# Kernel optimization log

Hardware: AMD Instinct MI355X
Metric: run time of the kernel (lower is better)

Reference implementation:

```python
import jax, jax.numpy as jnp
import numpy as np

B, T, D = 4, 2048, 512
H, HS = 8, 64            # n_head, head_size
E, K = 8, 2              # num_experts, top_k
CAP = int(B * T * K / E * 1.0)  # expert capacity = 2048
EPS = 1e-5


def setup_inputs() -> dict:
    key = jax.random.key(0)
    ks = jax.random.split(key, 16)
    s = lambda k, shp, fan: jax.random.normal(k, shp, jnp.float32) * (fan ** -0.5)
    return {
        "x": jax.random.normal(ks[0], (B, T, D), jnp.float32),
        "ln1_g": jnp.ones((D,), jnp.float32), "ln1_b": jnp.zeros((D,), jnp.float32),
        "Wq": s(ks[1], (H, D, HS), D), "Wk": s(ks[2], (H, D, HS), D), "Wv": s(ks[3], (H, D, HS), D),
        "Wo": s(ks[4], (D, D), D), "bo": jnp.zeros((D,), jnp.float32),
        "ln2_g": jnp.ones((D,), jnp.float32), "ln2_b": jnp.zeros((D,), jnp.float32),
        "Wg": s(ks[5], (D, E), D), "bg": jnp.zeros((E,), jnp.float32),
        "Wn": s(ks[6], (D, E), D), "bn": jnp.zeros((E,), jnp.float32),
        "W1": s(ks[7], (E, D, 4 * D), D), "b1": jnp.zeros((E, 4 * D), jnp.float32),
        "W2": s(ks[8], (E, 4 * D, D), 4 * D), "b2": jnp.zeros((E, D), jnp.float32),
    }


def _ln(x, g, b):
    m = jnp.mean(x, -1, keepdims=True)
    v = jnp.var(x, -1, keepdims=True)
    return (x - m) * jax.lax.rsqrt(v + EPS) * g + b


def _attn(h, Wq, Wk, Wv, Wo, bo):
    q = jnp.einsum('btd,hde->bhte', h, Wq)
    k = jnp.einsum('btd,hde->bhte', h, Wk)
    v = jnp.einsum('btd,hde->bhte', h, Wv)
    # NOTE: source scales by C**-0.5 with C = n_embed (not head_size)
    wei = jnp.einsum('bhte,bhse->bhts', q, k) * (D ** -0.5)
    causal = jnp.tril(jnp.ones((T, T), bool))
    wei = jnp.where(causal, wei, -jnp.inf)
    wei = jax.nn.softmax(wei, axis=-1)
    out = jnp.einsum('bhts,bhse->bhte', wei, v)              # [B,H,T,HS]
    out = out.transpose(0, 2, 1, 3).reshape(B, T, D)          # concat heads
    return out @ Wo + bo


def _moe(h, Wg, bg, Wn, bn, W1, b1, W2, b2):
    logits = h @ Wg + bg
    noise_logits = h @ Wn + bn
    noise = jax.random.normal(jax.random.key(42), logits.shape, logits.dtype) * jax.nn.softplus(noise_logits)
    noisy = logits + noise
    vals, idx = jax.lax.top_k(noisy, K)                       # [B,T,K]
    # softmax over -inf-masked sparse logits == softmax over top-k values, scattered
    gates = (jax.nn.softmax(vals, -1)[..., None] * jax.nn.one_hot(idx, E, dtype=h.dtype)).sum(-2)  # [B,T,E]
    flat_x = h.reshape(-1, D)
    flat_g = gates.reshape(-1, E)
    flat_idx = idx.reshape(-1, K)
    N = flat_x.shape[0]
    mask = (flat_idx[None] == jnp.arange(E)[:, None, None]).any(-1)   # [E,N]
    rank = jnp.cumsum(mask, axis=1) - 1
    keep = mask & (rank < CAP)                                 # first CAP tokens per expert
    slot = jnp.where(keep, rank, CAP)
    tok = jnp.arange(N, dtype=jnp.int32)

    def build(s, kp):
        buf = jnp.zeros(CAP + 1, jnp.int32).at[s].set(tok)
        vb = jnp.zeros(CAP + 1, bool).at[s].set(kp)
        return buf[:CAP], vb[:CAP]

    idx_buf, valid = jax.vmap(build)(slot, keep)               # [E,CAP]
    xg = flat_x[idx_buf]                                       # [E,CAP,D]
    mid = jax.nn.relu(jnp.einsum('ecd,edf->ecf', xg, W1) + b1[:, None, :])
    out = jnp.einsum('ecf,efd->ecd', mid, W2) + b2[:, None, :]
    gate_sel = flat_g[idx_buf, jnp.arange(E)[:, None]]         # [E,CAP]
    w = out * (gate_sel * valid.astype(h.dtype))[..., None]
    upd = jnp.zeros_like(flat_x).at[idx_buf.reshape(-1)].add(w.reshape(-1, D))
    return upd.reshape(h.shape)


def reference(x, ln1_g, ln1_b, Wq, Wk, Wv, Wo, bo, ln2_g, ln2_b,
              Wg, bg, Wn, bn, W1, b1, W2, b2):
    x = x + _attn(_ln(x, ln1_g, ln1_b), Wq, Wk, Wv, Wo, bo)
    x = x + _moe(_ln(x, ln2_g, ln2_b), Wg, bg, Wn, bn, W1, b1, W2, b2)
    return x
```

## Files before the change

kernel.cpp:

```cpp
#include <hip/hip_runtime.h>
#include <math.h>

#define TSEQ 2048
#define DD   512
#define NH   8
#define HSZ  64
#define NE   8
#define NTOK 8192
#define CAPK 2048
#define FF   2048

typedef __bf16 bf16x8 __attribute__((ext_vector_type(8)));
typedef float  f32x4  __attribute__((ext_vector_type(4)));
typedef unsigned int u32;
typedef u32 u32x2 __attribute__((ext_vector_type(2)));
typedef short s16x4 __attribute__((ext_vector_type(4)));

#define WAITVM(N) asm volatile("s_waitcnt vmcnt(" #N ")" ::: "memory")

__device__ __forceinline__ void gload16(const void* g, void* l){
  __builtin_amdgcn_global_load_lds((const __attribute__((address_space(1))) u32*)g,
                                   (__attribute__((address_space(3))) u32*)l, 16, 0, 0);
}

__device__ __forceinline__ u32 pkbf(float a, float b){
  unsigned short ua = __builtin_bit_cast(unsigned short, (__bf16)a);
  unsigned short ub = __builtin_bit_cast(unsigned short, (__bf16)b);
  return (u32)ua | ((u32)ub << 16);
}

__device__ __forceinline__ s16x4 mk4(u32 a, u32 b){
  u32x2 t; t[0] = a; t[1] = b;
  return __builtin_bit_cast(s16x4, t);
}

__device__ __forceinline__ unsigned rotl32(unsigned x, int r){ return (x<<r)|(x>>(32-r)); }

__device__ __forceinline__ void threefry2x32(unsigned c0, unsigned c1, unsigned &o0, unsigned &o1){
  const unsigned k0 = 0u, k1 = 42u;
  const unsigned k2 = k0 ^ k1 ^ 0x1BD11BDAu;
  unsigned x0 = c0 + k0, x1 = c1 + k1;
#define TFR(rot) { x0 += x1; x1 = rotl32(x1, rot); x1 ^= x0; }
  TFR(13) TFR(15) TFR(26) TFR(6)   x0 += k1; x1 += k2 + 1u;
  TFR(17) TFR(29) TFR(16) TFR(24)  x0 += k2; x1 += k0 + 2u;
  TFR(13) TFR(15) TFR(26) TFR(6)   x0 += k0; x1 += k1 + 3u;
  TFR(17) TFR(29) TFR(16) TFR(24)  x0 += k1; x1 += k2 + 4u;
  TFR(13) TFR(15) TFR(26) TFR(6)   x0 += k2; x1 += k0 + 5u;
#undef TFR
  o0 = x0; o1 = x1;
}

__device__ __forceinline__ float erfinv_f(float x){
  float w = -log1pf(-x*x);
  float p;
  if (w < 5.0f){
    w -= 2.5f;
    p = 2.81022636e-08f;
    p = fmaf(p,w, 3.43273939e-07f);
    p = fmaf(p,w,-3.5233877e-06f);
    p = fmaf(p,w,-4.39150654e-06f);
    p = fmaf(p,w, 0.00021858087f);
    p = fmaf(p,w,-0.00125372503f);
    p = fmaf(p,w,-0.00417768164f);
    p = fmaf(p,w, 0.246640727f);
    p = fmaf(p,w, 1.50140941f);
  } else {
    w = sqrtf(w) - 3.0f;
    p = -0.000200214257f;
    p = fmaf(p,w, 0.000100950558f);
    p = fmaf(p,w, 0.00134934322f);
    p = fmaf(p,w,-0.00367342844f);
    p = fmaf(p,w, 0.00573950773f);
    p = fmaf(p,w,-0.0076224613f);
    p = fmaf(p,w, 0.00943887047f);
    p = fmaf(p,w, 1.00167406f);
    p = fmaf(p,w, 2.83297682f);
  }
  return p * x;
}

__global__ __launch_bounds__(256) void ln_split(const float* __restrict__ x,
    const float* __restrict__ gw, const float* __restrict__ bw,
    __bf16* __restrict__ ohi, __bf16* __restrict__ olo)
{
  int row  = blockIdx.x*4 + threadIdx.y;
  int lane = threadIdx.x;
  const float* xr = x + (size_t)row*DD;
  float4 a = *(const float4*)(xr + lane*4);
  float4 c = *(const float4*)(xr + 256 + lane*4);
  float s  = a.x+a.y+a.z+a.w + c.x+c.y+c.z+c.w;
  float ss = a.x*a.x+a.y*a.y+a.z*a.z+a.w*a.w + c.x*c.x+c.y*c.y+c.z*c.z+c.w*c.w;
  #pragma unroll
  for (int off = 32; off; off >>= 1){ s += __shfl_xor(s, off); ss += __shfl_xor(ss, off); }
  float m   = s * (1.0f/DD);
  float var = ss * (1.0f/DD) - m*m;
  float r   = 1.0f / sqrtf(var + 1e-5f);
  float4 g1 = *(const float4*)(gw + lane*4);
  float4 b1 = *(const float4*)(bw + lane*4);
  float4 g2 = *(const float4*)(gw + 256 + lane*4);
  float4 b2 = *(const float4*)(bw + 256 + lane*4);
  float f1[4], f2[4];
  f1[0]=(a.x-m)*r*g1.x+b1.x; f1[1]=(a.y-m)*r*g1.y+b1.y; f1[2]=(a.z-m)*r*g1.z+b1.z; f1[3]=(a.w-m)*r*g1.w+b1.w;
  f2[0]=(c.x-m)*r*g2.x+b2.x; f2[1]=(c.y-m)*r*g2.y+b2.y; f2[2]=(c.z-m)*r*g2.z+b2.z; f2[3]=(c.w-m)*r*g2.w+b2.w;
  __bf16 h1v[4] __attribute__((aligned(8))), l1v[4] __attribute__((aligned(8)));
  __bf16 h2v[4] __attribute__((aligned(8))), l2v[4] __attribute__((aligned(8)));
  #pragma unroll
  for (int j = 0; j < 4; ++j){
    __bf16 hb = (__bf16)f1[j]; h1v[j]=hb; l1v[j]=(__bf16)(f1[j]-(float)hb);
    __bf16 hc = (__bf16)f2[j]; h2v[j]=hc; l2v[j]=(__bf16)(f2[j]-(float)hc);
  }
  size_t base = (size_t)row*DD + lane*4;
  *(uint2*)(ohi + base)       = *(const uint2*)h1v;
  *(uint2*)(olo + base)       = *(const uint2*)l1v;
  *(uint2*)(ohi + base + 256) = *(const uint2*)h2v;
  *(uint2*)(olo + base + 256) = *(const uint2*)l2v;
}

__global__ __launch_bounds__(256) void pack_qkv_split(const float* __restrict__ Wq,
    const float* __restrict__ Wk, const float* __restrict__ Wv,
    __bf16* __restrict__ dhi, __bf16* __restrict__ dlo)
{
  __shared__ float t[64][65];
  int z = blockIdx.y;
  int kt = blockIdx.x*64;
  int sel = z >> 3, hh = z & 7;
  const float* W = (sel==0 ? Wq : (sel==1 ? Wk : Wv)) + (size_t)hh*DD*HSZ;
  int tid = threadIdx.x;
  int r = tid>>2, c0 = (tid&3)*16;
  #pragma unroll
  for (int j = 0; j < 16; j += 4){
    float4 v = *(const float4*)&W[(size_t)(kt+r)*HSZ + c0 + j];
    t[r][c0+j]=v.x; t[r][c0+j+1]=v.y; t[r][c0+j+2]=v.z; t[r][c0+j+3]=v.w;
  }
  __syncthreads();
  __bf16 hb[16] __attribute__((aligned(32)));
  __bf16 lb[16] __attribute__((aligned(32)));
  #pragma unroll
  for (int j = 0; j < 16; ++j){
    float f = t[c0+j][r];
    __bf16 h = (__bf16)f; hb[j]=h; lb[j]=(__bf16)(f-(float)h);
  }
  size_t off = (size_t)(z*64 + r)*512 + kt + c0;
  *(uint4*)(dhi+off) = ((const uint4*)hb)[0]; *(uint4*)(dhi+off+8) = ((const uint4*)hb)[1];
  *(uint4*)(dlo+off) = ((const uint4*)lb)[0]; *(uint4*)(dlo+off+8) = ((const uint4*)lb)[1];
}

__global__ __launch_bounds__(256) void transp_split(const float* __restrict__ src,
    __bf16* __restrict__ dhi, __bf16* __restrict__ dlo, int Ms, int Ns)
{
  __shared__ float t[64][65];
  int nt = blockIdx.x*64, mt = blockIdx.y*64;
  int tid = threadIdx.x;
  int r = tid>>2, c0 = (tid&3)*16;
  #pragma unroll
  for (int j = 0; j < 16; j += 4){
    float4 v = *(const float4*)&src[(size_t)(mt+r)*Ns + nt + c0 + j];
    t[r][c0+j]=v.x; t[r][c0+j+1]=v.y; t[r][c0+j+2]=v.z; t[r][c0+j+3]=v.w;
  }
  __syncthreads();
  __bf16 hb[16] __attribute__((aligned(32)));
  __bf16 lb[16] __attribute__((aligned(32)));
  #pragma unroll
  for (int j = 0; j < 16; ++j){
    float f = t[c0+j][r];
    __bf16 h = (__bf16)f; hb[j]=h; lb[j]=(__bf16)(f-(float)h);
  }
  size_t off = (size_t)(nt + r)*Ms + mt + c0;
  *(uint4*)(dhi+off) = ((const uint4*)hb)[0]; *(uint4*)(dhi+off+8) = ((const uint4*)hb)[1];
  *(uint4*)(dlo+off) = ((const uint4*)lb)[0]; *(uint4*)(dlo+off+8) = ((const uint4*)lb)[1];
}

template<int BIAS, int RES>
__global__ __launch_bounds__(256) void gemm_mfma3(
    const __bf16* __restrict__ Ahi, const __bf16* __restrict__ Alo,
    const __bf16* __restrict__ Bhi, const __bf16* __restrict__ Blo,
    const float* __restrict__ bias, const float* __restrict__ res,
    float* __restrict__ C, int M, int N, int K)
{
  __shared__ __bf16 AsH[2][4096];
  __shared__ __bf16 AsL[2][4096];
  __shared__ __bf16 BsH[2][4096];
  __shared__ __bf16 BsL[2][4096];
  int m0 = blockIdx.y*128, n0 = blockIdx.x*128;
  int tid = threadIdx.x;
  int w = tid>>6, l = tid&63;
  int wm = w>>1, wn = w&1;
  int srow = w*32 + (l>>2);
  int skb  = (l&3)<<4;
  const char* agh = (const char*)(Ahi + (size_t)(m0+srow)*K) + skb;
  const char* agl = (const char*)(Alo + (size_t)(m0+srow)*K) + skb;
  const char* bgh = (const char*)(Bhi + (size_t)(n0+srow)*K) + skb;
  const char* bgl = (const char*)(Blo + (size_t)(n0+srow)*K) + skb;
  size_t r16 = (size_t)16*K*sizeof(__bf16);

  f32x4 acc[4][4] = {};
  int rl = l & 15, kh = l >> 4;
  const __bf16* abh = &AsH[0][(wm*64 + rl)*32 + kh*8];
  const __bf16* abl = &AsL[0][(wm*64 + rl)*32 + kh*8];
  const __bf16* bbh = &BsH[0][(wn*64 + rl)*32 + kh*8];
  const __bf16* bbl = &BsL[0][(wn*64 + rl)*32 + kh*8];

  auto STAGE = [&](int bb, int kt){
    size_t o = (size_t)kt*64;
    gload16(agh+o,     &AsH[bb][w*1024]);
    gload16(agh+o+r16, &AsH[bb][w*1024+512]);
    gload16(agl+o,     &AsL[bb][w*1024]);
    gload16(agl+o+r16, &AsL[bb][w*1024+512]);
    gload16(bgh+o,     &BsH[bb][w*1024]);
    gload16(bgh+o+r16, &BsH[bb][w*1024+512]);
    gload16(bgl+o,     &BsL[bb][w*1024]);
    gload16(bgl+o+r16, &BsL[bb][w*1024+512]);
  };

  int nkt = K >> 5;
  STAGE(0, 0);
  for (int kt = 0; kt < nkt; ++kt){
    int bb = kt & 1;
    if (kt + 1 < nkt){ STAGE(bb^1, kt+1); WAITVM(8); }
    else             { WAITVM(0); }
    __builtin_amdgcn_s_barrier();
    bf16x8 afh[4], afl[4], bfh[4], bfl[4];
    #pragma unroll
    for (int i = 0; i < 4; ++i){
      afh[i] = *(const bf16x8*)(abh + bb*4096 + i*512);
      afl[i] = *(const bf16x8*)(abl + bb*4096 + i*512);
      bfh[i] = *(const bf16x8*)(bbh + bb*4096 + i*512);
      bfl[i] = *(const bf16x8*)(bbl + bb*4096 + i*512);
    }
    #pragma unroll
    for (int fm = 0; fm < 4; ++fm)
      #pragma unroll
      for (int fn = 0; fn < 4; ++fn){
        acc[fm][fn] = __builtin_amdgcn_mfma_f32_16x16x32_bf16(afh[fm], bfl[fn], acc[fm][fn], 0, 0, 0);
        acc[fm][fn] = __builtin_amdgcn_mfma_f32_16x16x32_bf16(afl[fm], bfh[fn], acc[fm][fn], 0, 0, 0);
        acc[fm][fn] = __builtin_amdgcn_mfma_f32_16x16x32_bf16(afh[fm], bfh[fn], acc[fm][fn], 0, 0, 0);
      }
    __builtin_amdgcn_s_barrier();
  }

  int ccol = l & 15, cr = (l >> 4) * 4;
  #pragma unroll
  for (int fn = 0; fn < 4; ++fn){
    int n = n0 + wn*64 + fn*16 + ccol;
    float bv = BIAS ? bias[n] : 0.0f;
    #pragma unroll
    for (int fm = 0; fm < 4; ++fm){
      int mb = m0 + wm*64 + fm*16 + cr;
      #pragma unroll
      for (int r = 0; r < 4; ++r){
        float v = acc[fm][fn][r] + bv;
        if (RES) v += res[(size_t)(mb+r)*N + n];
        C[(size_t)(mb+r)*N + n] = v;
// ... 13 lines not shown
  int flat = blockIdx.x;
  int e = flat & ((1<<EBITS)-1);
  int tile = flat >> EBITS;
  int n0 = (tile & ((1<<LOGN)-1)) * 128;
  int m0 = (tile >> LOGN) * 128;
  const __bf16* Be = Bt + (size_t)e*N*K;
  const float*  be = bias + (size_t)e*N;
  int tid = threadIdx.x;
  int w = tid>>6, l = tid&63;
  int wm = w>>1, wn = w&1;
  int srow = w*32 + (l>>2);
  int skb  = (l&3)<<4;
  const char* ag;
  if (GATHER){
    int tok = idxb[e*CAPK + m0 + srow];
    ag = (const char*)(A + (size_t)tok*K) + skb;
  } else {
    ag = (const char*)(A + (size_t)e*M*K + (size_t)(m0 + srow)*K) + skb;
  }
  const char* bg = (const char*)(Be + (size_t)(n0 + srow)*K) + skb;
  size_t r16;
  if (GATHER){
    int tok2 = idxb[e*CAPK + m0 + srow + 16];
    r16 = (size_t)((const char*)(A + (size_t)tok2*K) + skb - ag);
  } else {
    r16 = (size_t)16*K*sizeof(__bf16);
  }

  f32x4 acc[4][4] = {};
  int rl = l & 15, kh = l >> 4;
  const __bf16* abase = &Asl[0][(wm*64 + rl)*32 + kh*8];
  const __bf16* bbase = &Bsl[0][(wn*64 + rl)*32 + kh*8];

  size_t br16 = (size_t)16*K*sizeof(__bf16);
  auto STAGE = [&](int bb, int kt){
    size_t o = (size_t)kt*64;
    gload16(ag+o,      &Asl[bb][w*1024]);
    gload16(ag+o+r16,  &Asl[bb][w*1024+512]);
    gload16(bg+o,      &Bsl[bb][w*1024]);
    gload16(bg+o+br16, &Bsl[bb][w*1024+512]);
  };

  int nkt = K >> 5;
  STAGE(0, 0);
  for (int kt = 0; kt < nkt; ++kt){
    int bb = kt & 1;
    if (kt + 1 < nkt){ STAGE(bb^1, kt+1); WAITVM(4); }
    else             { WAITVM(0); }
    __builtin_amdgcn_s_barrier();
    bf16x8 af[4], bf[4];
    #pragma unroll
    for (int i = 0; i < 4; ++i){
      af[i] = *(const bf16x8*)(abase + bb*4096 + i*512);
      bf[i] = *(const bf16x8*)(bbase + bb*4096 + i*512);
    }
    #pragma unroll
    for (int fm = 0; fm < 4; ++fm)
      #pragma unroll
      for (int fn = 0; fn < 4; ++fn)
        acc[fm][fn] = __builtin_amdgcn_mfma_f32_16x16x32_bf16(af[fm], bf[fn], acc[fm][fn], 0, 0, 0);
    __builtin_amdgcn_s_barrier();
  }

  int ccol = l & 15, cr = (l >> 4) * 4;
  char* Ce = (char*)Cv + (size_t)e*M*N*(STORE_BF16 ? 2 : 4);
  #pragma unroll
  for (int fn = 0; fn < 4; ++fn){
    int n = n0 + wn*64 + fn*16 + ccol;
    float bv = be[n];
    #pragma unroll
    for (int fm = 0; fm < 4; ++fm){
      int mb = m0 + wm*64 + fm*16 + cr;
      #pragma unroll
      for (int r = 0; r < 4; ++r){
        float v = acc[fm][fn][r] + bv;
        if (RELU) v = fmaxf(v, 0.f);
        if (STORE_BF16) ((__bf16*)Ce)[(size_t)(mb+r)*N + n] = (__bf16)v;
        else            ((float*)Ce)[(size_t)(mb+r)*N + n] = v;
      }
    }
  }
}

__global__ __launch_bounds__(256) void transp_conv(const float* __restrict__ src,
    __bf16* __restrict__ dst, int Ms, int Ns)
{
  __shared__ __bf16 t[64][72];
  int e = blockIdx.z;
  const float* s = src + (size_t)e*Ms*Ns;
  __bf16* d = dst + (size_t)e*Ms*Ns;
  int mt = blockIdx.y*64, nt = blockIdx.x*64;
  int tid = threadIdx.x;
  int r = tid>>2, c0 = (tid&3)*16;
  #pragma unroll
  for (int j = 0; j < 16; j += 4){
    float4 v = *(const float4*)&s[(size_t)(mt+r)*Ns + nt + c0 + j];
    t[r][c0+j]   = (__bf16)v.x; t[r][c0+j+1] = (__bf16)v.y;
    t[r][c0+j+2] = (__bf16)v.z; t[r][c0+j+3] = (__bf16)v.w;
  }
  __syncthreads();
  __bf16 tmp[16] __attribute__((aligned(32)));
  #pragma unroll
  for (int j = 0; j < 16; ++j) tmp[j] = t[c0+j][r];
  uint4* dp = (uint4*)&d[(size_t)(nt+r)*Ms + mt + c0];
  dp[0] = ((const uint4*)tmp)[0];
  dp[1] = ((const uint4*)tmp)[1];
}

__global__ __launch_bounds__(256) void convert_kv(const float* __restrict__ qkv,
    __bf16* __restrict__ khi, __bf16* __restrict__ klo,
    __bf16* __restrict__ vthi, __bf16* __restrict__ vtlo)
{
  int t0 = blockIdx.x*64;
  int bh = blockIdx.y;
  int b = bh >> 3, h = bh & 7;
  int tid = threadIdx.x;
  {
    int r = tid >> 2, e0 = (tid & 3) * 16;
    const float* src = qkv + ((size_t)(b*TSEQ + t0 + r))*1536 + 512 + h*64 + e0;
    __bf16 hi[16] __attribute__((aligned(16)));
    __bf16 lo[16] __attribute__((aligned(16)));
    #pragma unroll
    for (int j = 0; j < 16; j += 4){
      float4 v = *(const float4*)(src + j);
      float f[4] = {v.x, v.y, v.z, v.w};
      #pragma unroll
      for (int q = 0; q < 4; ++q){
        __bf16 hb = (__bf16)f[q];
        hi[j+q] = hb; lo[j+q] = (__bf16)(f[q] - (float)hb);
      }
    }
    size_t off = ((size_t)(bh*TSEQ + t0 + r))*64 + e0;
    *(uint4*)(khi + off)     = ((const uint4*)hi)[0];
    *(uint4*)(khi + off + 8) = ((const uint4*)hi)[1];
    *(uint4*)(klo + off)     = ((const uint4*)lo)[0];
    *(uint4*)(klo + off + 8) = ((const uint4*)lo)[1];
  }
  {
    int key0 = (tid & 15) * 4, e0 = (tid >> 4) * 4;
    float4 v[4];
    #pragma unroll
    for (int j = 0; j < 4; ++j)
      v[j] = *(const float4*)(qkv + ((size_t)(b*TSEQ + t0 + key0 + j))*1536 + 1024 + h*64 + e0);
    float col[4][4];
    col[0][0]=v[0].x; col[0][1]=v[1].x; col[0][2]=v[2].x; col[0][3]=v[3].x;
    col[1][0]=v[0].y; col[1][1]=v[1].y; col[1][2]=v[2].y; col[1][3]=v[3].y;
    col[2][0]=v[0].z; col[2][1]=v[1].z; col[2][2]=v[2].z; col[2][3]=v[3].z;
    col[3][0]=v[0].w; col[3][1]=v[1].w; col[3][2]=v[2].w; col[3][3]=v[3].w;
    #pragma unroll
    for (int kk = 0; kk < 4; ++kk){
      __bf16 hi[4] __attribute__((aligned(8)));
      __bf16 lo[4] __attribute__((aligned(8)));
      #pragma unroll
      for (int j = 0; j < 4; ++j){
        __bf16 hb = (__bf16)col[kk][j];
        hi[j] = hb; lo[j] = (__bf16)(col[kk][j] - (float)hb);
      }
      size_t off = ((size_t)(bh*64 + e0 + kk))*TSEQ + t0 + key0;
      *(uint2*)(vthi + off) = *(const uint2*)hi;
      *(uint2*)(vtlo + off) = *(const uint2*)lo;
    }
  }
}

__global__ __launch_bounds__(512) void attn_mfma(const float* __restrict__ qkv,
    const __bf16* __restrict__ khi_g, const __bf16* __restrict__ klo_g,
    const __bf16* __restrict__ vthi_g, const __bf16* __restrict__ vtlo_g,
    __bf16* __restrict__ ahi, __bf16* __restrict__ alo)
{
  __shared__ __align__(16) char ldsbuf[65536];
  int bh = blockIdx.x;
  int qtA = blockIdx.y, qtB = 15 - qtA;
  int b = bh >> 3, h = bh & 7;
  int tid = threadIdx.x;
  int w = tid >> 6, l = tid & 63;
  int g = l >> 4, r = l & 15;
  const float qsc = 0.04419417382415922f * 1.4426950408889634f;

  int qb[2]; qb[0] = qtA*128 + w*16; qb[1] = qtB*128 + (7-w)*16;
  int kdiag[2]; kdiag[0] = qb[0] >> 6; kdiag[1] = qb[1] >> 6;

  bf16x8 qhi[2][2], qlo[2][2];
  #pragma unroll
  for (int qf = 0; qf < 2; ++qf)
    #pragma unroll
    for (int ks = 0; ks < 2; ++ks){
      const float* src = qkv + ((size_t)(b*TSEQ + qb[qf] + r))*1536 + h*64 + ks*32 + g*8;
      float4 v0 = *(const float4*)src;
      float4 v1 = *(const float4*)(src + 4);
      float f[8] = {v0.x,v0.y,v0.z,v0.w,v1.x,v1.y,v1.z,v1.w};
      bf16x8 hi, lo;
      #pragma unroll
      for (int i = 0; i < 8; ++i){
        float fs = f[i] * qsc;
        __bf16 hb = (__bf16)fs;
        hi[i] = hb; lo[i] = (__bf16)(fs - (float)hb);
      }
      qhi[qf][ks] = hi; qlo[qf][ks] = lo;
    }

  f32x4 ot[4][2] = {};
  float m_r[2] = {-INFINITY, -INFINITY};
  float l_r[2] = {0.f, 0.f};

  int nkt = 2*qtB + 2;
  size_t kbase = (size_t)bh*TSEQ*64;
  size_t vbase = (size_t)bh*64*TSEQ;

  auto STAGE = [&](int buf, int kt){
    int row = tid >> 3, cc = tid & 7;
    int sw = (cc ^ (row & 7)) * 8;
    char* d = ldsbuf + buf*32768 + (w << 10);
    gload16(khi_g  + kbase + (size_t)(kt*64 + row)*64 + sw, d);
    gload16(klo_g  + kbase + (size_t)(kt*64 + row)*64 + sw, d + 8192);
    gload16(vthi_g + vbase + (size_t)row*TSEQ + kt*64 + sw,  d + 16384);
    gload16(vtlo_g + vbase + (size_t)row*TSEQ + kt*64 + sw,  d + 24576);
  };

  STAGE(0, 0);

  for (int kt = 0; kt < nkt; ++kt){
    int buf = kt & 1;
    if (kt + 1 < nkt){ STAGE(buf ^ 1, kt + 1); WAITVM(4); }
    else             { WAITVM(0); }
    __builtin_amdgcn_s_barrier();

    bool act[2];
    act[0] = (kt <= kdiag[0]);
    act[1] = (kt <= kdiag[1]);

    const char* K0 = ldsbuf + buf*32768;
    const char* K1 = K0 + 8192;
    const char* V0 = K0 + 16384;
    const char* V1 = K0 + 24576;

    f32x4 s[4][2] = {};
    #pragma unroll
    for (int kf = 0; kf < 4; ++kf){
      int rowk = kf*16 + r;
      int rsw = (rowk & 7) << 4;
      #pragma unroll
      for (int ks = 0; ks < 2; ++ks){
        int off = rowk*128 + ((((ks*4 + g) << 4)) ^ rsw);
        bf16x8 khf = *(const bf16x8*)(K0 + off);
        bf16x8 klf = *(const bf16x8*)(K1 + off);
        #pragma unroll
        for (int qf = 0; qf < 2; ++qf){
          if (act[qf]){
            s[kf][qf] = __builtin_amdgcn_mfma_f32_16x16x32_bf16(khf, qlo[qf][ks], s[kf][qf], 0,0,0);
            s[kf][qf] = __builtin_amdgcn_mfma_f32_16x16x32_bf16(klf, qhi[qf][ks], s[kf][qf], 0,0,0);
            s[kf][qf] = __builtin_amdgcn_mfma_f32_16x16x32_bf16(khf, qhi[qf][ks], s[kf][qf], 0,0,0);
          }
        }
      }
    }

    u32 phi[4][2][2], plo[4][2][2];
    #pragma unroll
    for (int qf = 0; qf < 2; ++qf){
      if (act[qf]){
        int q = qb[qf] + r;
        float p[4][4];
        float mx = -INFINITY;
        if (kt == kdiag[qf]){
          #pragma unroll
          for (int kf = 0; kf < 4; ++kf)
            #pragma unroll
            for (int e = 0; e < 4; ++e){
              int key = kt*64 + kf*16 + g*4 + e;
              float sv = (key <= q) ? s[kf][qf][e] : -INFINITY;
              p[kf][e] = sv;
              mx = fmaxf(mx, sv);
            }
        } else {
          #pragma unroll
          for (int kf = 0; kf < 4; ++kf)
            #pragma unroll
            for (int e = 0; e < 4; ++e){
              float sv = s[kf][qf][e];
              p[kf][e] = sv;
              mx = fmaxf(mx, sv);
            }
        }
        mx = fmaxf(mx, __shfl_xor(mx, 16));
        mx = fmaxf(mx, __shfl_xor(mx, 32));
        if (__any(mx > m_r[qf])){
          float mn = fmaxf(m_r[qf], mx);
          float fj = exp2f(m_r[qf] - mn);
          m_r[qf] = mn;
          l_r[qf] *= fj;
          #pragma unroll
          for (int ef = 0; ef < 4; ++ef)
            #pragma unroll
            for (int e = 0; e < 4; ++e)
              ot[ef][qf][e] *= fj;
        }
        float ts = 0.f;
        #pragma unroll
        for (int kf = 0; kf < 4; ++kf)
          #pragma unroll
          for (int e = 0; e < 4; ++e){
            float pv = exp2f(p[kf][e] - m_r[qf]);
            p[kf][e] = pv; ts += pv;
          }
        ts += __shfl_xor(ts, 16); ts += __shfl_xor(ts, 32);
        l_r[qf] += ts;
        #pragma unroll
        for (int kf = 0; kf < 4; ++kf){
          __bf16 h0=(__bf16)p[kf][0], h1=(__bf16)p[kf][1], h2=(__bf16)p[kf][2], h3=(__bf16)p[kf][3];
          phi[kf][qf][0] = pkbf(p[kf][0], p[kf][1]);
          phi[kf][qf][1] = pkbf(p[kf][2], p[kf][3]);
          plo[kf][qf][0] = pkbf(p[kf][0]-(float)h0, p[kf][1]-(float)h1);
          plo[kf][qf][1] = pkbf(p[kf][2]-(float)h2, p[kf][3]-(float)h3);
        }
      }
    }

    #pragma unroll
    for (int kf = 0; kf < 4; ++kf){
      #pragma unroll
      for (int ef = 0; ef < 4; ++ef){
        int rowv = ef*16 + r;
        int off = rowv*128 + ((((2*kf + (g>>1)) ^ (rowv & 7)) << 4)) + (g&1)*8;
        s16x4 vh = *(const s16x4*)(V0 + off);
        s16x4 vl = *(const s16x4*)(V1 + off);
        #pragma unroll
        for (int qf = 0; qf < 2; ++qf){
          if (act[qf]){
            s16x4 ph = mk4(phi[kf][qf][0], phi[kf][qf][1]);
            s16x4 pl = mk4(plo[kf][qf][0], plo[kf][qf][1]);
            ot[ef][qf] = __builtin_amdgcn_mfma_f32_16x16x16bf16_1k(vh, pl, ot[ef][qf], 0,0,0);
            ot[ef][qf] = __builtin_amdgcn_mfma_f32_16x16x16bf16_1k(vl, ph, ot[ef][qf], 0,0,0);
            ot[ef][qf] = __builtin_amdgcn_mfma_f32_16x16x16bf16_1k(vh, ph, ot[ef][qf], 0,0,0);
          }
        }
      }
    }
    __builtin_amdgcn_s_barrier();
  }

  float* Osh = (float*)ldsbuf;
  #pragma unroll
  for (int qf = 0; qf < 2; ++qf){
    float inv = 1.0f / l_r[qf];
    int qloc = (qf ? (7-w) : w)*16 + r;
    #pragma unroll
    for (int ef = 0; ef < 4; ++ef)
      #pragma unroll
      for (int e = 0; e < 4; ++e)
        Osh[qloc*68 + ef*16 + g*4 + e] = ot[ef][qf][e] * inv;
    __syncthreads();
    {
      int qt = qf ? qtB : qtA;
      int q = tid >> 2, e0 = (tid & 3)*16;
      const float* srow = Osh + q*68 + e0;
      size_t base = ((size_t)(b*TSEQ + qt*128 + q))*DD + h*64 + e0;
      #pragma unroll
      for (int j = 0; j < 4; ++j){
        float4 v = *(const float4*)(srow + j*4);
        float f[4] = {v.x, v.y, v.z, v.w};
        __bf16 hb[4] __attribute__((aligned(8)));
        __bf16 lb[4] __attribute__((aligned(8)));
        #pragma unroll
        for (int q2 = 0; q2 < 4; ++q2){
          __bf16 h2b = (__bf16)f[q2];
          hb[q2] = h2b; lb[q2] = (__bf16)(f[q2] - (float)h2b);
        }
        *(uint2*)(ahi + base + j*4) = *(const uint2*)hb;
        *(uint2*)(alo + base + j*4) = *(const uint2*)lb;
      }
    }
    __syncthreads();
  }
}

__global__ __launch_bounds__(256) void routerln_kernel(const float* __restrict__ x1,
    const float* __restrict__ gw, const float* __restrict__ bw,
    const float* __restrict__ Wg, const float* __restrict__ bg,
    const float* __restrict__ Wn, const float* __restrict__ bn,
    __bf16* __restrict__ h2b,
    int* __restrict__ idx0, int* __restrict__ idx1,
    float* __restrict__ g0, float* __restrict__ g1)
{
  int wid = threadIdx.x >> 6, lane = threadIdx.x & 63;
  int tok = blockIdx.x*4 + wid;
  const float* xr = x1 + (size_t)tok*DD;
  float4 a = *(const float4*)(xr + lane*4);
  float4 c = *(const float4*)(xr + 256 + lane*4);
  float s  = a.x+a.y+a.z+a.w + c.x+c.y+c.z+c.w;
  float ss = a.x*a.x+a.y*a.y+a.z*a.z+a.w*a.w + c.x*c.x+c.y*c.y+c.z*c.z+c.w*c.w;
  #pragma unroll
  for (int off = 32; off; off >>= 1){ s += __shfl_xor(s, off); ss += __shfl_xor(ss, off); }
  float m   = s * (1.0f/DD);
  float var = ss * (1.0f/DD) - m*m;
  float rr  = 1.0f / sqrtf(var + 1e-5f);
  float4 g1v = *(const float4*)(gw + lane*4);
  float4 b1v = *(const float4*)(bw + lane*4);
  float4 g2v = *(const float4*)(gw + 256 + lane*4);
  float4 b2v = *(const float4*)(bw + 256 + lane*4);
  float f1[4], f2[4];
  f1[0]=(a.x-m)*rr*g1v.x+b1v.x; f1[1]=(a.y-m)*rr*g1v.y+b1v.y; f1[2]=(a.z-m)*rr*g1v.z+b1v.z; f1[3]=(a.w-m)*rr*g1v.w+b1v.w;
  f2[0]=(c.x-m)*rr*g2v.x+b2v.x; f2[1]=(c.y-m)*rr*g2v.y+b2v.y; f2[2]=(c.z-m)*rr*g2v.z+b2v.z; f2[3]=(c.w-m)*rr*g2v.w+b2v.w;
  {
    __bf16 h1v[4] __attribute__((aligned(8)));
    __bf16 h2v[4] __attribute__((aligned(8)));
    #pragma unroll
    for (int j = 0; j < 4; ++j){ h1v[j] = (__bf16)f1[j]; h2v[j] = (__bf16)f2[j]; }
    size_t base = (size_t)tok*DD + lane*4;
    *(uint2*)(h2b + base)       = *(const uint2*)h1v;
    *(uint2*)(h2b + base + 256) = *(const uint2*)h2v;
  }
  float ag[8] = {0,0,0,0,0,0,0,0}, an[8] = {0,0,0,0,0,0,0,0};
  int d1 = lane*4, d2 = 256 + lane*4;
// ... 41 lines not shown
    float dexp = expf(v1 - v0);
    float ssum = 1.0f + dexp;
    idx0[tok] = i0; idx1[tok] = i1;
    g0[tok] = 1.0f/ssum; g1[tok] = dexp/ssum;
  }
}

__global__ __launch_bounds__(256) void route_scan(const int* __restrict__ idx0,
    const int* __restrict__ idx1, int* __restrict__ idx_buf, int* __restrict__ tok_slot)
{
  int e = blockIdx.x, tid = threadIdx.x;
  for (int i = tid; i < CAPK; i += 256) idx_buf[e*CAPK + i] = 0;
  __syncthreads();
  int base = tid * 32;
  int cnt = 0;
  for (int j = 0; j < 32; ++j){ int t = base + j; cnt += (idx0[t]==e || idx1[t]==e) ? 1 : 0; }
  __shared__ int ps[256];
  ps[tid] = cnt; __syncthreads();
  for (int off = 1; off < 256; off <<= 1){
    int add = (tid >= off) ? ps[tid - off] : 0;
    __syncthreads();
    ps[tid] += add;
    __syncthreads();
  }
  int slot = ps[tid] - cnt;
  for (int j = 0; j < 32; ++j){
    int t = base + j;
    int k = (idx0[t]==e) ? 0 : ((idx1[t]==e) ? 1 : -1);
    if (k >= 0){
      if (slot < CAPK){ idx_buf[e*CAPK + slot] = t; tok_slot[t*2 + k] = slot; }
      else            { tok_slot[t*2 + k] = -1; }
      slot++;
    }
  }
}

__global__ __launch_bounds__(128) void combine_kernel(const float* __restrict__ x1,
    const __bf16* __restrict__ eout, const int* __restrict__ idx0, const int* __restrict__ idx1,
    const float* __restrict__ g0, const float* __restrict__ g1,
    const int* __restrict__ tok_slot, float* __restrict__ outp)
{
  int n = blockIdx.x, t = threadIdx.x;
  float4 acc = *(const float4*)(x1 + (size_t)n*DD + t*4);
  #pragma unroll
  for (int k = 0; k < 2; ++k){
    int s = tok_slot[n*2 + k];
    if (s >= 0){
      int e  = (k==0) ? idx0[n] : idx1[n];
      float g = (k==0) ? g0[n] : g1[n];
      __bf16 vb[4] __attribute__((aligned(8)));
      *(uint2*)vb = *(const uint2*)(eout + ((size_t)(e*CAPK + s))*DD + t*4);
      acc.x = fmaf(g, (float)vb[0], acc.x); acc.y = fmaf(g, (float)vb[1], acc.y);
      acc.z = fmaf(g, (float)vb[2], acc.z); acc.w = fmaf(g, (float)vb[3], acc.w);
    }
  }
  *(float4*)(outp + (size_t)n*DD + t*4) = acc;
}

extern "C" void kernel_launch(void* const* d_in, const int* in_sizes, int n_in,
                              void* d_out, int out_size, void* d_ws, size_t ws_size,
                              hipStream_t stream)
{
  const float* x    = (const float*)d_in[0];
  const float* ln1g = (const float*)d_in[1];
  const float* ln1b = (const float*)d_in[2];
  const float* Wq   = (const float*)d_in[3];
  const float* Wk   = (const float*)d_in[4];
  const float* Wv   = (const float*)d_in[5];
  const float* Wo   = (const float*)d_in[6];
  const float* bo   = (const float*)d_in[7];
  const float* ln2g = (const float*)d_in[8];
  const float* ln2b = (const float*)d_in[9];
  const float* Wg   = (const float*)d_in[10];
  const float* bg   = (const float*)d_in[11];
  const float* Wn   = (const float*)d_in[12];
  const float* bn   = (const float*)d_in[13];
  const float* W1   = (const float*)d_in[14];
  const float* b1   = (const float*)d_in[15];
  const float* W2   = (const float*)d_in[16];
  const float* b2   = (const float*)d_in[17];
  float* out = (float*)d_out;
  char* ws = (char*)d_ws;
  const size_t MB = 1u << 20;

  __bf16* h1hi   = (__bf16*)(ws);
  __bf16* h1lo   = (__bf16*)(ws + 8*MB);
  __bf16* attnhi = (__bf16*)(ws);
  __bf16* attnlo = (__bf16*)(ws + 8*MB);
  __bf16* h2b    = (__bf16*)(ws);
  float*  qkv    = (float*)(ws + 16*MB);
  __bf16* W1T    = (__bf16*)(ws + 16*MB);
  __bf16* W2T    = (__bf16*)(ws + 32*MB);
  __bf16* eoutb  = (__bf16*)(ws + 48*MB);
  float*  x1     = (float*)(ws + 64*MB);
  __bf16* Khi    = (__bf16*)(ws + 80*MB);
  __bf16* Klo    = (__bf16*)(ws + 88*MB);
  __bf16* Vthi   = (__bf16*)(ws + 96*MB);
  __bf16* Vtlo   = (__bf16*)(ws + 104*MB);
  __bf16* Bqh    = (__bf16*)(ws + 80*MB);
  __bf16* Bql    = (__bf16*)(ws + 82*MB);
  __bf16* mid    = (__bf16*)(ws + 80*MB);
  __bf16* WoTh   = (__bf16*)(ws + 144*MB);
  __bf16* WoTl   = (__bf16*)(ws + 144*MB + 512*1024);
  char*   smallp = ws + 145*MB;
  int*   idx0     = (int*)smallp;
  int*   idx1     = idx0 + NTOK;
  float* g0       = (float*)(idx1 + NTOK);
  float* g1       = g0 + NTOK;
  int*   tok_slot = (int*)(g1 + NTOK);
  int*   idx_buf  = tok_slot + NTOK*2;

  ln_split<<<dim3(NTOK/4), dim3(64,4), 0, stream>>>(x, ln1g, ln1b, h1hi, h1lo);
  pack_qkv_split<<<dim3(8,24), 256, 0, stream>>>(Wq, Wk, Wv, Bqh, Bql);
  transp_split<<<dim3(8,8), 256, 0, stream>>>(Wo, WoTh, WoTl, DD, DD);
  gemm_mfma3<0,0><<<dim3(12,64), 256, 0, stream>>>(h1hi, h1lo, Bqh, Bql, nullptr, nullptr, qkv, NTOK, 1536, DD);
  convert_kv<<<dim3(TSEQ/64, 32), 256, 0, stream>>>(qkv, Khi, Klo, Vthi, Vtlo);
  attn_mfma<<<dim3(32, 8), 512, 0, stream>>>(qkv, Khi, Klo, Vthi, Vtlo, attnhi, attnlo);
  gemm_mfma3<1,1><<<dim3(4,64), 256, 0, stream>>>(attnhi, attnlo, WoTh, WoTl, bo, x, x1, NTOK, DD, DD);
  routerln_kernel<<<dim3(NTOK/4), 256, 0, stream>>>(x1, ln2g, ln2b, Wg, bg, Wn, bn,
      h2b, idx0, idx1, g0, g1);
  transp_conv<<<dim3(32,8,NE), 256, 0, stream>>>(W1, W1T, DD, FF);
  transp_conv<<<dim3(8,32,NE), 256, 0, stream>>>(W2, W2T, FF, DD);
  route_scan<<<dim3(NE), 256, 0, stream>>>(idx0, idx1, idx_buf, tok_slot);
  gemm_mfma<1,1,1,4,3><<<dim3(8*16*16), 256, 0, stream>>>(
      h2b, W1T, b1, mid, idx_buf, CAPK, FF, DD);
  gemm_mfma<1,0,0,2,3><<<dim3(8*16*4), 256, 0, stream>>>(
      mid, W2T, b2, eoutb, nullptr, CAPK, DD, FF);
  combine_kernel<<<dim3(NTOK), 128, 0, stream>>>(x1, eoutb, idx0, idx1, g0, g1, tok_slot, out);
}
```

Baseline: 385.9 us.

## Use 128-key attention tiles with dynamic LDS and merge prep kernels

The attention kernel now stages 128 keys per iteration instead of 64. That halves the number of loop trips, barriers and softmax rescales, and needs 128KB of dynamic LDS set through hipFuncSetAttribute. The LayerNorm and the QKV/Wo weight packing are merged into one launch, and the W1/W2 transposes into another, to cut launch overhead. The larger tile uses more registers and LDS, which may lower occupancy, and it computes more masked work on the diagonal tile.

```diff
diff --git a/kernel.cpp b/kernel.cpp
--- a/kernel.cpp
+++ b/kernel.cpp
@@ -79,95 +79,92 @@
   return p * x;
 }
 
-__global__ __launch_bounds__(256) void ln_split(const float* __restrict__ x,
-    const float* __restrict__ gw, const float* __restrict__ bw,
-    __bf16* __restrict__ ohi, __bf16* __restrict__ olo)
-{
-  int row  = blockIdx.x*4 + threadIdx.y;
-  int lane = threadIdx.x;
-  const float* xr = x + (size_t)row*DD;
-  float4 a = *(const float4*)(xr + lane*4);
-  float4 c = *(const float4*)(xr + 256 + lane*4);
-  float s  = a.x+a.y+a.z+a.w + c.x+c.y+c.z+c.w;
-  float ss = a.x*a.x+a.y*a.y+a.z*a.z+a.w*a.w + c.x*c.x+c.y*c.y+c.z*c.z+c.w*c.w;
-  #pragma unroll
-  for (int off = 32; off; off >>= 1){ s += __shfl_xor(s, off); ss += __shfl_xor(ss, off); }
-  float m   = s * (1.0f/DD);
-  float var = ss * (1.0f/DD) - m*m;
-  float r   = 1.0f / sqrtf(var + 1e-5f);
-  float4 g1 = *(const float4*)(gw + lane*4);
-  float4 b1 = *(const float4*)(bw + lane*4);
-  float4 g2 = *(const float4*)(gw + 256 + lane*4);
-  float4 b2 = *(const float4*)(bw + 256 + lane*4);
-  float f1[4], f2[4];
-  f1[0]=(a.x-m)*r*g1.x+b1.x; f1[1]=(a.y-m)*r*g1.y+b1.y; f1[2]=(a.z-m)*r*g1.z+b1.z; f1[3]=(a.w-m)*r*g1.w+b1.w;
-  f2[0]=(c.x-m)*r*g2.x+b2.x; f2[1]=(c.y-m)*r*g2.y+b2.y; f2[2]=(c.z-m)*r*g2.z+b2.z; f2[3]=(c.w-m)*r*g2.w+b2.w;
-  __bf16 h1v[4] __attribute__((aligned(8))), l1v[4] __attribute__((aligned(8)));
-  __bf16 h2v[4] __attribute__((aligned(8))), l2v[4] __attribute__((aligned(8)));
-  #pragma unroll
-  for (int j = 0; j < 4; ++j){
-    __bf16 hb = (__bf16)f1[j]; h1v[j]=hb; l1v[j]=(__bf16)(f1[j]-(float)hb);
-    __bf16 hc = (__bf16)f2[j]; h2v[j]=hc; l2v[j]=(__bf16)(f2[j]-(float)hc);
-  }
-  size_t base = (size_t)row*DD + lane*4;
-  *(uint2*)(ohi + base)       = *(const uint2*)h1v;
-  *(uint2*)(olo + base)       = *(const uint2*)l1v;
-  *(uint2*)(ohi + base + 256) = *(const uint2*)h2v;
-  *(uint2*)(olo + base + 256) = *(const uint2*)l2v;
-}
-
-__global__ __launch_bounds__(256) void pack_qkv_split(const float* __restrict__ Wq,
-    const float* __restrict__ Wk, const float* __restrict__ Wv,
-    __bf16* __restrict__ dhi, __bf16* __restrict__ dlo)
+__global__ __launch_bounds__(256) void prep_kernel(
+    const float* __restrict__ x, const float* __restrict__ ln1g, const float* __restrict__ ln1b,
+    __bf16* __restrict__ h1hi, __bf16* __restrict__ h1lo,
+    const float* __restrict__ Wq, const float* __restrict__ Wk, const float* __restrict__ Wv,
+    __bf16* __restrict__ Bqh, __bf16* __restrict__ Bql,
+    const float* __restrict__ Wo, __bf16* __restrict__ WoTh, __bf16* __restrict__ WoTl)
 {
   __shared__ float t[64][65];
-  int z = blockIdx.y;
-  int kt = blockIdx.x*64;
-  int sel = z >> 3, hh = z & 7;
-  const float* W = (sel==0 ? Wq : (sel==1 ? Wk : Wv)) + (size_t)hh*DD*HSZ;
+  int blk = blockIdx.x;
   int tid = threadIdx.x;
-  int r = tid>>2, c0 = (tid&3)*16;
-  #pragma unroll
-  for (int j = 0; j < 16; j += 4){
-    float4 v = *(const float4*)&W[(size_t)(kt+r)*HSZ + c0 + j];
-    t[r][c0+j]=v.x; t[r][c0+j+1]=v.y; t[r][c0+j+2]=v.z; t[r][c0+j+3]=v.w;
-  }
-  __syncthreads();
-  __bf16 hb[16] __attribute__((aligned(32)));
-  __bf16 lb[16] __attribute__((aligned(32)));
-  #pragma unroll
-  for (int j = 0; j < 16; ++j){
-    float f = t[c0+j][r];
-    __bf16 h = (__bf16)f; hb[j]=h; lb[j]=(__bf16)(f-(float)h);
-  }
-  size_t off = (size_t)(z*64 + r)*512 + kt + c0;
-  *(uint4*)(dhi+off) = ((const uint4*)hb)[0]; *(uint4*)(dhi+off+8) = ((const uint4*)hb)[1];
-  *(uint4*)(dlo+off) = ((const uint4*)lb)[0]; *(uint4*)(dlo+off+8) = ((const uint4*)lb)[1];
-}
-
-__global__ __launch_bounds__(256) void transp_split(const float* __restrict__ src,
-    __bf16* __restrict__ dhi, __bf16* __restrict__ dlo, int Ms, int Ns)
-{
-  __shared__ float t[64][65];
-  int nt = blockIdx.x*64, mt = blockIdx.y*64;
-  int tid = threadIdx.x;
-  int r = tid>>2, c0 = (tid&3)*16;
-  #pragma unroll
-  for (int j = 0; j < 16; j += 4){
-    float4 v = *(const float4*)&src[(size_t)(mt+r)*Ns + nt + c0 + j];
-    t[r][c0+j]=v.x; t[r][c0+j+1]=v.y; t[r][c0+j+2]=v.z; t[r][c0+j+3]=v.w;
-  }
-  __syncthreads();
-  __bf16 hb[16] __attribute__((aligned(32)));
-  __bf16 lb[16] __attribute__((aligned(32)));
-  #pragma unroll
-  for (int j = 0; j < 16; ++j){
-    float f = t[c0+j][r];
-    __bf16 h = (__bf16)f; hb[j]=h; lb[j]=(__bf16)(f-(float)h);
-  }
-  size_t off = (size_t)(nt + r)*Ms + mt + c0;
-  *(uint4*)(dhi+off) = ((const uint4*)hb)[0]; *(uint4*)(dhi+off+8) = ((const uint4*)hb)[1];
-  *(uint4*)(dlo+off) = ((const uint4*)lb)[0]; *(uint4*)(dlo+off+8) = ((const uint4*)lb)[1];
+  if (blk < 2048){
+    int row  = blk*4 + (tid >> 6);
+    int lane = tid & 63;
+    const float* xr = x + (size_t)row*DD;
+    float4 a = *(const float4*)(xr + lane*4);
+    float4 c = *(const float4*)(xr + 256 + lane*4);
+    float s  = a.x+a.y+a.z+a.w + c.x+c.y+c.z+c.w;
+    float ss = a.x*a.x+a.y*a.y+a.z*a.z+a.w*a.w + c.x*c.x+c.y*c.y+c.z*c.z+c.w*c.w;
+    #pragma unroll
+    for (int off = 32; off; off >>= 1){ s += __shfl_xor(s, off); ss += __shfl_xor(ss, off); }
+    float m   = s * (1.0f/DD);
+    float var = ss * (1.0f/DD) - m*m;
+    float r   = 1.0f / sqrtf(var + 1e-5f);
+    float4 g1 = *(const float4*)(ln1g + lane*4);
+    float4 b1 = *(const float4*)(ln1b + lane*4);
+    float4 g2 = *(const float4*)(ln1g + 256 + lane*4);
+    float4 b2 = *(const float4*)(ln1b + 256 + lane*4);
+    float f1[4], f2[4];
+    f1[0]=(a.x-m)*r*g1.x+b1.x; f1[1]=(a.y-m)*r*g1.y+b1.y; f1[2]=(a.z-m)*r*g1.z+b1.z; f1[3]=(a.w-m)*r*g1.w+b1.w;
+    f2[0]=(c.x-m)*r*g2.x+b2.x; f2[1]=(c.y-m)*r*g2.y+b2.y; f2[2]=(c.z-m)*r*g2.z+b2.z; f2[3]=(c.w-m)*r*g2.w+b2.w;
+    __bf16 h1v[4] __attribute__((aligned(8))), l1v[4] __attribute__((aligned(8)));
+    __bf16 h2v[4] __attribute__((aligned(8))), l2v[4] __attribute__((aligned(8)));
+    #pragma unroll
+    for (int j = 0; j < 4; ++j){
+      __bf16 hb = (__bf16)f1[j]; h1v[j]=hb; l1v[j]=(__bf16)(f1[j]-(float)hb);
+      __bf16 hc = (__bf16)f2[j]; h2v[j]=hc; l2v[j]=(__bf16)(f2[j]-(float)hc);
+    }
+    size_t base = (size_t)row*DD + lane*4;
+    *(uint2*)(h1hi + base)       = *(const uint2*)h1v;
+    *(uint2*)(h1lo + base)       = *(const uint2*)l1v;
+    *(uint2*)(h1hi + base + 256) = *(const uint2*)h2v;
+    *(uint2*)(h1lo + base + 256) = *(const uint2*)l2v;
+  } else if (blk < 2240){
+    int bx = blk - 2048;
+    int kt = (bx & 7) * 64;
+    int z  = bx >> 3;
+    int sel = z >> 3, hh = z & 7;
+    const float* W = (sel==0 ? Wq : (sel==1 ? Wk : Wv)) + (size_t)hh*DD*HSZ;
+    int r = tid>>2, c0 = (tid&3)*16;
+    #pragma unroll
+    for (int j = 0; j < 16; j += 4){
+      float4 v = *(const float4*)&W[(size_t)(kt+r)*HSZ + c0 + j];
+      t[r][c0+j]=v.x; t[r][c0+j+1]=v.y; t[r][c0+j+2]=v.z; t[r][c0+j+3]=v.w;
+    }
+    __syncthreads();
+    __bf16 hb[16] __attribute__((aligned(32)));
+    __bf16 lb[16] __attribute__((aligned(32)));
+    #pragma unroll
+    for (int j = 0; j < 16; ++j){
+      float f = t[c0+j][r];
+      __bf16 h = (__bf16)f; hb[j]=h; lb[j]=(__bf16)(f-(float)h);
+    }
+    size_t off = (size_t)(z*64 + r)*512 + kt + c0;
+    *(uint4*)(Bqh+off) = ((const uint4*)hb)[0]; *(uint4*)(Bqh+off+8) = ((const uint4*)hb)[1];
+    *(uint4*)(Bql+off) = ((const uint4*)lb)[0]; *(uint4*)(Bql+off+8) = ((const uint4*)lb)[1];
+  } else {
+    int bx = blk - 2240;
+    int nt = (bx & 7) * 64, mt = (bx >> 3) * 64;
+    int r = tid>>2, c0 = (tid&3)*16;
+    #pragma unroll
+    for (int j = 0; j < 16; j += 4){
+      float4 v = *(const float4*)&Wo[(size_t)(mt+r)*DD + nt + c0 + j];
+      t[r][c0+j]=v.x; t[r][c0+j+1]=v.y; t[r][c0+j+2]=v.z; t[r][c0+j+3]=v.w;
+    }
+    __syncthreads();
+    __bf16 hb[16] __attribute__((aligned(32)));
+    __bf16 lb[16] __attribute__((aligned(32)));
+    #pragma unroll
+    for (int j = 0; j < 16; ++j){
+      float f = t[c0+j][r];
+      __bf16 h = (__bf16)f; hb[j]=h; lb[j]=(__bf16)(f-(float)h);
+    }
+    size_t off = (size_t)(nt + r)*DD + mt + c0;
+    *(uint4*)(WoTh+off) = ((const uint4*)hb)[0]; *(uint4*)(WoTh+off+8) = ((const uint4*)hb)[1];
+    *(uint4*)(WoTl+off) = ((const uint4*)lb)[0]; *(uint4*)(WoTl+off+8) = ((const uint4*)lb)[1];
+  }
 }
 
 template<int BIAS, int RES>
@@ -347,14 +344,17 @@
   }
 }
 
-__global__ __launch_bounds__(256) void transp_conv(const float* __restrict__ src,
-    __bf16* __restrict__ dst, int Ms, int Ns)
+__global__ __launch_bounds__(256) void transp_conv2(const float* __restrict__ W1,
+    const float* __restrict__ W2, __bf16* __restrict__ d1, __bf16* __restrict__ d2)
 {
   __shared__ __bf16 t[64][72];
   int e = blockIdx.z;
-  const float* s = src + (size_t)e*Ms*Ns;
-  __bf16* d = dst + (size_t)e*Ms*Ns;
-  int mt = blockIdx.y*64, nt = blockIdx.x*64;
+  int id = blockIdx.x;
+  const float* s; __bf16* d; int Ms, Ns, mt, nt;
+  if (id < 256){ s = W1; d = d1; Ms = DD; Ns = FF; nt = (id&31)*64; mt = (id>>5)*64; }
+  else { int i2 = id-256; s = W2; d = d2; Ms = FF; Ns = DD; nt = (i2&7)*64; mt = (i2>>3)*64; }
+  s += (size_t)e*Ms*Ns;
+  d += (size_t)e*Ms*Ns;
   int tid = threadIdx.x;
   int r = tid>>2, c0 = (tid&3)*16;
   #pragma unroll
@@ -433,7 +433,7 @@
     const __bf16* __restrict__ vthi_g, const __bf16* __restrict__ vtlo_g,
     __bf16* __restrict__ ahi, __bf16* __restrict__ alo)
 {
-  __shared__ __align__(16) char ldsbuf[65536];
+  extern __shared__ __align__(16) char ldsbuf[];
   int bh = blockIdx.x;
   int qtA = blockIdx.y, qtB = 15 - qtA;
   int b = bh >> 3, h = bh & 7;
@@ -443,7 +443,7 @@
   const float qsc = 0.04419417382415922f * 1.4426950408889634f;
 
   int qb[2]; qb[0] = qtA*128 + w*16; qb[1] = qtB*128 + (7-w)*16;
-  int kdiag[2]; kdiag[0] = qb[0] >> 6; kdiag[1] = qb[1] >> 6;
+  int kdiag[2]; kdiag[0] = qtA; kdiag[1] = qtB;
 
   bf16x8 qhi[2][2], qlo[2][2];
   #pragma unroll
@@ -468,40 +468,46 @@
   float m_r[2] = {-INFINITY, -INFINITY};
   float l_r[2] = {0.f, 0.f};
 
-  int nkt = 2*qtB + 2;
+  int nkt = qtB + 1;
   size_t kbase = (size_t)bh*TSEQ*64;
   size_t vbase = (size_t)bh*64*TSEQ;
 
   auto STAGE = [&](int buf, int kt){
     int row = tid >> 3, cc = tid & 7;
-    int sw = (cc ^ (row & 7)) * 8;
-    char* d = ldsbuf + buf*32768 + (w << 10);
-    gload16(khi_g  + kbase + (size_t)(kt*64 + row)*64 + sw, d);
-    gload16(klo_g  + kbase + (size_t)(kt*64 + row)*64 + sw, d + 8192);
-    gload16(vthi_g + vbase + (size_t)row*TSEQ + kt*64 + sw,  d + 16384);
-    gload16(vtlo_g + vbase + (size_t)row*TSEQ + kt*64 + sw,  d + 24576);
+    char* base = ldsbuf + buf*65536 + (w << 10);
+    #pragma unroll
+    for (int p = 0; p < 2; ++p){
+      int krow = p*64 + row;
+      int ksw = (cc ^ (krow & 7)) * 8;
+      gload16(khi_g + kbase + (size_t)(kt*128 + krow)*64 + ksw, base + p*8192);
+      gload16(klo_g + kbase + (size_t)(kt*128 + krow)*64 + ksw, base + 16384 + p*8192);
+      int vch = p*8 + cc;
+      int vsw = ((vch ^ (row & 7)) & 15) * 8;
+      gload16(vthi_g + vbase + (size_t)row*TSEQ + kt*128 + vsw, base + 32768 + p*8192);
+      gload16(vtlo_g + vbase + (size_t)row*TSEQ + kt*128 + vsw, base + 49152 + p*8192);
+    }
   };
 
   STAGE(0, 0);
 
   for (int kt = 0; kt < nkt; ++kt){
     int buf = kt & 1;
-    if (kt + 1 < nkt){ STAGE(buf ^ 1, kt + 1); WAITVM(4); }
+    if (kt + 1 < nkt){ STAGE(buf ^ 1, kt + 1); WAITVM(8); }
     else             { WAITVM(0); }
     __builtin_amdgcn_s_barrier();
 
     bool act[2];
     act[0] = (kt <= kdiag[0]);
-    act[1] = (kt <= kdiag[1]);
-
-    const char* K0 = ldsbuf + buf*32768;
-    const char* K1 = K0 + 8192;
-    const char* V0 = K0 + 16384;
-    const char* V1 = K0 + 24576;
-
-    f32x4 s[4][2] = {};
-    #pragma unroll
-    for (int kf = 0; kf < 4; ++kf){
+    act[1] = true;
+
+    const char* K0 = ldsbuf + buf*65536;
+    const char* K1 = K0 + 16384;
+    const char* V0 = K0 + 32768;
+    const char* V1 = K0 + 49152;
+
+    f32x4 s[8][2] = {};
+    #pragma unroll
+    for (int kf = 0; kf < 8; ++kf){
       int rowk = kf*16 + r;
       int rsw = (rowk & 7) << 4;
       #pragma unroll
@@ -520,32 +526,27 @@
       }
     }
 
-    u32 phi[4][2][2], plo[4][2][2];
     #pragma unroll
     for (int qf = 0; qf < 2; ++qf){
       if (act[qf]){
         int q = qb[qf] + r;
-        float p[4][4];
         float mx = -INFINITY;
         if (kt == kdiag[qf]){
           #pragma unroll
-          for (int kf = 0; kf < 4; ++kf)
+          for (int kf = 0; kf < 8; ++kf)
             #pragma unroll
             for (int e = 0; e < 4; ++e){
-              int key = kt*64 + kf*16 + g*4 + e;
+              int key = kt*128 + kf*16 + g*4 + e;
               float sv = (key <= q) ? s[kf][qf][e] : -INFINITY;
-              p[kf][e] = sv;
+              s[kf][qf][e] = sv;
               mx = fmaxf(mx, sv);
             }
         } else {
           #pragma unroll
-          for (int kf = 0; kf < 4; ++kf)
+          for (int kf = 0; kf < 8; ++kf)
             #pragma unroll
-            for (int e = 0; e < 4; ++e){
-              float sv = s[kf][qf][e];
-              p[kf][e] = sv;
-              mx = fmaxf(mx, sv);
-            }
+            for (int e = 0; e < 4; ++e)
+              mx = fmaxf(mx, s[kf][qf][e]);
         }
         mx = fmaxf(mx, __shfl_xor(mx, 16));
         mx = fmaxf(mx, __shfl_xor(mx, 32));
@@ -562,38 +563,45 @@
         }
         float ts = 0.f;
         #pragma unroll
-        for (int kf = 0; kf < 4; ++kf)
+        for (int kf = 0; kf < 8; ++kf)
           #pragma unroll
           for (int e = 0; e < 4; ++e){
-            float pv = exp2f(p[kf][e] - m_r[qf]);
-            p[kf][e] = pv; ts += pv;
+            float pv = exp2f(s[kf][qf][e] - m_r[qf]);
+            s[kf][qf][e] = pv; ts += pv;
           }
         ts += __shfl_xor(ts, 16); ts += __shfl_xor(ts, 32);
         l_r[qf] += ts;
-        #pragma unroll
-        for (int kf = 0; kf < 4; ++kf){
-          __bf16 h0=(__bf16)p[kf][0], h1=(__bf16)p[kf][1], h2=(__bf16)p[kf][2], h3=(__bf16)p[kf][3];
-          phi[kf][qf][0] = pkbf(p[kf][0], p[kf][1]);
-          phi[kf][qf][1] = pkbf(p[kf][2], p[kf][3]);
-          plo[kf][qf][0] = pkbf(p[kf][0]-(float)h0, p[kf][1]-(float)h1);
-          plo[kf][qf][1] = pkbf(p[kf][2]-(float)h2, p[kf][3]-(float)h3);
+      }
+    }
+
+    #pragma unroll
+    for (int kf = 0; kf < 8; ++kf){
+      u32 PH[2][2], PL[2][2];
+      #pragma unroll
+      for (int qf = 0; qf < 2; ++qf){
+        if (act[qf]){
+          float p0 = s[kf][qf][0], p1 = s[kf][qf][1], p2 = s[kf][qf][2], p3 = s[kf][qf][3];
+          __bf16 h0=(__bf16)p0, h1=(__bf16)p1, h2=(__bf16)p2, h3=(__bf16)p3;
+          PH[qf][0] = pkbf(p0, p1);
+          PH[qf][1] = pkbf(p2, p3);
+          PL[qf][0] = pkbf(p0-(float)h0, p1-(float)h1);
+          PL[qf][1] = pkbf(p2-(float)h2, p3-(float)h3);
         }
       }
-    }
-
-    #pragma unroll
-    for (int kf = 0; kf < 4; ++kf){
+      int chunk = 2*kf + (g>>1);
+      int pb = (chunk >> 3) << 13;
+      int cl = chunk & 7;
       #pragma unroll
       for (int ef = 0; ef < 4; ++ef){
         int rowv = ef*16 + r;
-        int off = rowv*128 + ((((2*kf + (g>>1)) ^ (rowv & 7)) << 4)) + (g&1)*8;
+        int off = pb + rowv*128 + ((cl ^ (rowv & 7)) << 4) + (g&1)*8;
         s16x4 vh = *(const s16x4*)(V0 + off);
         s16x4 vl = *(const s16x4*)(V1 + off);
         #pragma unroll
         for (int qf = 0; qf < 2; ++qf){
           if (act[qf]){
-            s16x4 ph = mk4(phi[kf][qf][0], phi[kf][qf][1]);
-            s16x4 pl = mk4(plo[kf][qf][0], plo[kf][qf][1]);
+            s16x4 ph = mk4(PH[qf][0], PH[qf][1]);
+            s16x4 pl = mk4(PL[qf][0], PL[qf][1]);
             ot[ef][qf] = __builtin_amdgcn_mfma_f32_16x16x16bf16_1k(vh, pl, ot[ef][qf], 0,0,0);
             ot[ef][qf] = __builtin_amdgcn_mfma_f32_16x16x16bf16_1k(vl, ph, ot[ef][qf], 0,0,0);
             ot[ef][qf] = __builtin_amdgcn_mfma_f32_16x16x16bf16_1k(vh, ph, ot[ef][qf], 0,0,0);
@@ -801,6 +809,9 @@
   float* out = (float*)d_out;
   char* ws = (char*)d_ws;
   const size_t MB = 1u << 20;
+
+  (void)hipFuncSetAttribute((const void*)attn_mfma,
+      hipFuncAttributeMaxDynamicSharedMemorySize, 131072);
 
   __bf16* h1hi   = (__bf16*)(ws);
   __bf16* h1lo   = (__bf16*)(ws + 8*MB);
@@ -829,17 +840,15 @@
   int*   tok_slot = (int*)(g1 + NTOK);
   int*   idx_buf  = tok_slot + NTOK*2;
 
-  ln_split<<<dim3(NTOK/4), dim3(64,4), 0, stream>>>(x, ln1g, ln1b, h1hi, h1lo);
-  pack_qkv_split<<<dim3(8,24), 256, 0, stream>>>(Wq, Wk, Wv, Bqh, Bql);
-  transp_split<<<dim3(8,8), 256, 0, stream>>>(Wo, WoTh, WoTl, DD, DD);
+  prep_kernel<<<dim3(2304), 256, 0, stream>>>(x, ln1g, ln1b, h1hi, h1lo,
+      Wq, Wk, Wv, Bqh, Bql, Wo, WoTh, WoTl);
   gemm_mfma3<0,0><<<dim3(12,64), 256, 0, stream>>>(h1hi, h1lo, Bqh, Bql, nullptr, nullptr, qkv, NTOK, 1536, DD);
   convert_kv<<<dim3(TSEQ/64, 32), 256, 0, stream>>>(qkv, Khi, Klo, Vthi, Vtlo);
-  attn_mfma<<<dim3(32, 8), 512, 0, stream>>>(qkv, Khi, Klo, Vthi, Vtlo, attnhi, attnlo);
+  attn_mfma<<<dim3(32, 8), 512, 131072, stream>>>(qkv, Khi, Klo, Vthi, Vtlo, attnhi, attnlo);
   gemm_mfma3<1,1><<<dim3(4,64), 256, 0, stream>>>(attnhi, attnlo, WoTh, WoTl, bo, x, x1, NTOK, DD, DD);
   routerln_kernel<<<dim3(NTOK/4), 256, 0, stream>>>(x1, ln2g, ln2b, Wg, bg, Wn, bn,
       h2b, idx0, idx1, g0, g1);
-  transp_conv<<<dim3(32,8,NE), 256, 0, stream>>>(W1, W1T, DD, FF);
-  transp_conv<<<dim3(8,32,NE), 256, 0, stream>>>(W2, W2T, FF, DD);
+  transp_conv2<<<dim3(512,1,NE), 256, 0, stream>>>(W1, W2, W1T, W2T);
   route_scan<<<dim3(NE), 256, 0, stream>>>(idx0, idx1, idx_buf, tok_slot);
   gemm_mfma<1,1,1,4,3><<<dim3(8*16*16), 256, 0, stream>>>(
       h2b, W1T, b1, mid, idx_buf, CAPK, FF, DD);
```

Result: faster. 367.1 us (-4.9%).
